# Optimization experiments

Measured on AMD Instinct MI355X. Metric: run time of the kernel, lower is better.

The kernel has to match this reference:

```python
import jax, jax.numpy as jnp
import numpy as np

N = 100000   # total nodes across all graphs
E = 1600000  # edges (avg degree 16)
D = 128      # input feature dim
H = 64       # hidden dim
B = 8        # number of graphs
EPS = 1e-5   # BatchNorm eps


def setup_inputs() -> dict:
    key = jax.random.key(0)
    ks = jax.random.split(key, 12)
    x = jax.random.normal(ks[0], (N, D), dtype=jnp.float32)
    edge_index = jax.random.randint(ks[1], (2, E), 0, N, dtype=jnp.int64)
    batch = jnp.sort(jax.random.randint(ks[2], (N,), 0, B, dtype=jnp.int64))
    s1 = 1.0 / np.sqrt(D)
    s2 = 1.0 / np.sqrt(H)
    W1l = jax.random.uniform(ks[3], (D, H), minval=-s1, maxval=s1, dtype=jnp.float32)
    W1r = jax.random.uniform(ks[4], (D, H), minval=-s1, maxval=s1, dtype=jnp.float32)
    b1 = jnp.zeros((H,), jnp.float32)
    gamma1 = jnp.ones((H,), jnp.float32)
    beta1 = jnp.zeros((H,), jnp.float32)
    W2l = jax.random.uniform(ks[5], (H, H), minval=-s2, maxval=s2, dtype=jnp.float32)
    W2r = jax.random.uniform(ks[6], (H, H), minval=-s2, maxval=s2, dtype=jnp.float32)
    b2 = jnp.zeros((H,), jnp.float32)
    return {"x": x, "edge_index": edge_index, "batch": batch,
            "W1l": W1l, "b1": b1, "W1r": W1r, "gamma1": gamma1, "beta1": beta1,
            "W2l": W2l, "b2": b2, "W2r": W2r}


def _seg_mean(vals, idx, num):
    # scatter-mean: sum per segment / count, zero-degree segments give 0 (count clamped)
    s = jax.ops.segment_sum(vals, idx, num_segments=num)
    cnt = jax.ops.segment_sum(jnp.ones((idx.shape[0], 1), vals.dtype), idx, num_segments=num)
    return s / jnp.maximum(cnt, 1.0)


def reference(x, edge_index, batch, W1l, b1, W1r, gamma1, beta1, W2l, b2, W2r):
    src, dst = edge_index[0], edge_index[1]
    # SAGEConv layer 1: mean-aggregate neighbors, lin_l(agg) + lin_r(x)
    agg1 = _seg_mean(x[src], dst, N)            # [N, D]
    h = agg1 @ W1l + b1 + x @ W1r               # [N, H]
    # BatchNorm1d (training-mode batch stats, biased var) then ReLU
    mu = jnp.mean(h, axis=0)
    var = jnp.var(h, axis=0)
    h = (h - mu) * jax.lax.rsqrt(var + EPS) * gamma1 + beta1
    h = jax.nn.relu(h)
    # SAGEConv layer 2 (no norm/act after last layer)
    agg2 = _seg_mean(h[src], dst, N)            # [N, H]
    h2 = agg2 @ W2l + b2 + h @ W2r              # [N, H]
    # per-graph global mean pool -> [B, H]
    return _seg_mean(h2, batch, B)
```

## Files before the change

kernel.cpp:

```cpp
#include <hip/hip_runtime.h>

#define N_NODES 100000
#define E_EDGES 1600000
#define DIM 128
#define HID 64
#define NGRAPH 8
#define EPSBN 1e-5f

#define GSHIFT 9
#define GNODES (1 << GSHIFT)
#define NGROUP ((N_NODES + GNODES - 1) >> GSHIFT)
#define GCAP 10240
#define CHUNK 2048
#define PBLK 256
#define EPT (CHUNK / PBLK)
#define NCHUNK ((E_EDGES + CHUNK - 1) / CHUNK)
#define MM1B ((N_NODES + 63) / 64)
#define GATB 2048

#if __has_builtin(__builtin_amdgcn_cvt_pk_fp8_f32) && \
    __has_builtin(__builtin_amdgcn_cvt_pk_f32_fp8)
#define HW_FP8 1
#else
#define HW_FP8 0
#endif

typedef float floatx2 __attribute__((ext_vector_type(2)));

__device__ __forceinline__ unsigned f2bf_pack(float lo, float hi) {
  unsigned ul = __float_as_uint(lo);
  unsigned uh = __float_as_uint(hi);
  ul = (ul + 0x7fffu + ((ul >> 16) & 1u)) >> 16;
  uh = (uh + 0x7fffu + ((uh >> 16) & 1u)) >> 16;
  return (uh << 16) | ul;
}
__device__ __forceinline__ float bflo(unsigned u) {
  return __uint_as_float(u << 16);
}
__device__ __forceinline__ float bfhi(unsigned u) {
  return __uint_as_float(u & 0xffff0000u);
}

#if !HW_FP8
__device__ __forceinline__ unsigned char f32_to_e4m3(float f) {
  unsigned u = __float_as_uint(f);
  unsigned s = (u >> 24) & 0x80u;
  float a = fabsf(f);
  if (a >= 464.f) return (unsigned char)(s | 0x7E);
  if (a < 0.015625f) {
    int m = (int)rintf(a * 512.f);
    if (m >= 8) return (unsigned char)(s | 0x08);
    return (unsigned char)(s | (unsigned)m);
  }
  int e = (int)((u >> 23) & 0xFF) - 127;
  float q = ldexpf(a, -e) * 8.f;
  int m = (int)rintf(q);
  if (m == 16) { m = 8; ++e; }
  if (e > 8) return (unsigned char)(s | 0x7E);
  return (unsigned char)(s | (unsigned)(((e + 7) << 3) | (m - 8)));
}
#endif

__device__ __forceinline__ unsigned pack4_e4m3(float a, float b, float c,
                                               float d) {
#if HW_FP8
  int w = __builtin_amdgcn_cvt_pk_fp8_f32(a, b, 0, false);
  w = __builtin_amdgcn_cvt_pk_fp8_f32(c, d, w, true);
  return (unsigned)w;
#else
  return (unsigned)f32_to_e4m3(a) | ((unsigned)f32_to_e4m3(b) << 8) |
         ((unsigned)f32_to_e4m3(c) << 16) | ((unsigned)f32_to_e4m3(d) << 24);
#endif
}

__global__ __launch_bounds__(PBLK) void part_mm1_kernel(
    const int* __restrict__ src, const int* __restrict__ dst,
    int* __restrict__ gcnt, unsigned* __restrict__ part,
    const float* __restrict__ x, const float* __restrict__ W1l,
    const float* __restrict__ W1r, unsigned char* __restrict__ y1f8,
    unsigned* __restrict__ y2bf) {
  __shared__ __align__(16) unsigned char smraw[32768];

  if (blockIdx.x < NCHUNK) {
    int* hist = (int*)(smraw);
    int* sc = (int*)(smraw + 1024);
    int* scanoff = (int*)(smraw + 2048);
    int* gbase = (int*)(smraw + 3072);
    unsigned* buf = (unsigned*)(smraw + 4096);
    unsigned char* gid = smraw + 12288;

    int c = blockIdx.x;
    int e0 = c * CHUNK;
    int m = E_EDGES - e0;
    m = m < CHUNK ? m : CHUNK;
    int t = threadIdx.x;

    hist[t] = 0;
    __syncthreads();

    int myg[EPT];
    unsigned mytok[EPT];
    int myrank[EPT];
    #pragma unroll
    for (int q = 0; q < EPT; ++q) {
      int i = t + q * PBLK;
      if (i < m) {
        int d = dst[e0 + i];
        int s = src[e0 + i];
        int g = d >> GSHIFT;
        myg[q] = g;
        mytok[q] = ((unsigned)(d & (GNODES - 1)) << 17) | (unsigned)s;
        myrank[q] = atomicAdd(&hist[g], 1);
      } else {
        myg[q] = -1;
      }
    }
    __syncthreads();

    sc[t] = hist[t];
    if (t < NGROUP && hist[t] > 0) gbase[t] = atomicAdd(&gcnt[t], hist[t]);
    __syncthreads();
    for (int off = 1; off < 256; off <<= 1) {
      int add = (t >= off) ? sc[t - off] : 0;
      __syncthreads();
      sc[t] += add;
      __syncthreads();
    }
    scanoff[t] = sc[t] - hist[t];
    __syncthreads();

    #pragma unroll
    for (int q = 0; q < EPT; ++q) {
      if (myg[q] >= 0) {
        int pos = scanoff[myg[q]] + myrank[q];
        buf[pos] = mytok[q];
        gid[pos] = (unsigned char)myg[q];
      }
    }
    __syncthreads();

    for (int i = t; i < m; i += PBLK) {
      int g = gid[i];
      int addr = gbase[g] + (i - scanoff[g]);
      if (addr < GCAP) part[(size_t)g * GCAP + addr] = buf[i];
    }
  } else {
    float* xlds = (float*)smraw;
    int t = threadIdx.x;
    int brow = (blockIdx.x - NCHUNK) * 64;

    for (int i = t; i < 64 * 32; i += PBLK) {
      int r = i >> 5;
      int c4 = (i & 31) << 2;
      int n = brow + r;
      if (n < N_NODES) {
        float4 v = *reinterpret_cast<const float4*>(x + (size_t)n * DIM + c4);
        int w = c4 ^ ((r & 7) << 2);
        *reinterpret_cast<float4*>(xlds + r * DIM + w) = v;
      }
    }
    __syncthreads();

    int lane = t & 63;
    int c0 = __builtin_amdgcn_readfirstlane((int)(t >> 6) << 4);
    int n = brow + lane;
    if (n >= N_NODES) return;
    const float* xr = xlds + lane * DIM;
    int sw = (lane & 7) << 2;

    float a1[16], a2[16];
    #pragma unroll
    for (int j = 0; j < 16; ++j) { a1[j] = 0.f; a2[j] = 0.f; }

    for (int k = 0; k < DIM; k += 4) {
      float4 xv = *reinterpret_cast<const float4*>(xr + (k ^ sw));
      float xs[4] = {xv.x, xv.y, xv.z, xv.w};
      #pragma unroll
      for (int kk = 0; kk < 4; ++kk) {
        const float* w1 = W1l + (size_t)(k + kk) * HID + c0;
        const float* w2 = W1r + (size_t)(k + kk) * HID + c0;
        float xk = xs[kk];
        #pragma unroll
        for (int j = 0; j < 16; ++j) {
          a1[j] = fmaf(xk, w1[j], a1[j]);
          a2[j] = fmaf(xk, w2[j], a2[j]);
        }
      }
    }
    uint4 pk;
    pk.x = pack4_e4m3(a1[0], a1[1], a1[2], a1[3]);
    pk.y = pack4_e4m3(a1[4], a1[5], a1[6], a1[7]);
    pk.z = pack4_e4m3(a1[8], a1[9], a1[10], a1[11]);
    pk.w = pack4_e4m3(a1[12], a1[13], a1[14], a1[15]);
    *reinterpret_cast<uint4*>(y1f8 + (size_t)n * HID + c0) = pk;

    uint4 q0, q1;
    q0.x = f2bf_pack(a2[0], a2[1]);
    q0.y = f2bf_pack(a2[2], a2[3]);
    q0.z = f2bf_pack(a2[4], a2[5]);
    q0.w = f2bf_pack(a2[6], a2[7]);
    q1.x = f2bf_pack(a2[8], a2[9]);
    q1.y = f2bf_pack(a2[10], a2[11]);
    q1.z = f2bf_pack(a2[12], a2[13]);
    q1.w = f2bf_pack(a2[14], a2[15]);
    unsigned* ob = y2bf + (size_t)n * (HID / 2) + (c0 >> 1);
    reinterpret_cast<uint4*>(ob)[0] = q0;
    reinterpret_cast<uint4*>(ob)[1] = q1;
  }
}

__global__ __launch_bounds__(512) void groupcsr_kernel(
    const int* __restrict__ gcnt, const unsigned* __restrict__ part,
    const int* __restrict__ batch, int* __restrict__ rowptr,
    int* __restrict__ csr, unsigned* __restrict__ tok2) {
  __shared__ int hist[GNODES];
  __shared__ int excl[GNODES];
  __shared__ int degl[GNODES];
  __shared__ int batl[GNODES];
  __shared__ int sc2[256];
  int g = blockIdx.x;
  int t = threadIdx.x;

  if (t < 256) sc2[t] = (t < NGROUP) ? min(gcnt[t], GCAP) : 0;
  __syncthreads();
  for (int off = 1; off < 256; off <<= 1) {
    int add = (t < 256 && t >= off) ? sc2[t - off] : 0;
    __syncthreads();
    if (t < 256) sc2[t] += add;
    __syncthreads();
  }
  int gbase = (g > 0) ? sc2[g - 1] : 0;

  hist[t] = 0;
  {
    int n = (g << GSHIFT) + t;
    batl[t] = (n < N_NODES) ? batch[n] : 0;
  }
  __syncthreads();

  int cnt = min(gcnt[g], GCAP);
  const unsigned* ga = part + (size_t)g * GCAP;
  for (int i = t; i < cnt; i += 512) atomicAdd(&hist[ga[i] >> 17], 1);
  __syncthreads();

  int orig = hist[t];
  degl[t] = orig;
  for (int off = 1; off < GNODES; off <<= 1) {
    int add = (t >= off) ? hist[t - off] : 0;
    __syncthreads();
    hist[t] += add;
    __syncthreads();
  }
  excl[t] = hist[t] - orig;
  __syncthreads();

  int n = (g << GSHIFT) + t;
  if (n <= N_NODES) rowptr[n] = gbase + excl[t];
  if (g == 0 && t == 0) rowptr[0] = 0;
  __syncthreads();

  for (int i = t; i < cnt; i += 512) {
    unsigned p = ga[i];
    int dloc = (int)(p >> 17);
    int pos = gbase + atomicAdd(&excl[dloc], 1);
    unsigned s = p & 0x1FFFFu;
    csr[pos] = (int)s;
    unsigned dg = (unsigned)degl[dloc];
    if (dg > 1023u) dg = 1023u;
    tok2[pos] = (dg << 20) | ((unsigned)batl[dloc] << 17) | s;
  }
}

__global__ __launch_bounds__(PBLK) void part2_gather_kernel(
    const unsigned* __restrict__ tok2, int* __restrict__ gcnt2,
    unsigned* __restrict__ part2, const uint2* __restrict__ yf8,
    const int* __restrict__ csr, const int* __restrict__ rowptr,
    const unsigned* __restrict__ otherbf, const float* __restrict__ bias,
    unsigned* __restrict__ outCbf, float* __restrict__ stats) {
  __shared__ int hist[256];
  __shared__ int sc[256];
  __shared__ int scanoff[256];
  __shared__ int gbase[256];
  __shared__ unsigned buf[CHUNK];
  __shared__ unsigned char gid[CHUNK];
  __shared__ float ss[HID];
  __shared__ float sq[HID];

  if (blockIdx.x < NCHUNK) {
    int c = blockIdx.x;
    int e0 = c * CHUNK;
    int m = E_EDGES - e0;
    m = m < CHUNK ? m : CHUNK;
    int t = threadIdx.x;

    hist[t] = 0;
    __syncthreads();

    int myg[EPT];
    unsigned mytok[EPT];
    int myrank[EPT];
    #pragma unroll
    for (int q = 0; q < EPT; ++q) {
      int i = t + q * PBLK;
      if (i < m) {
        unsigned p = tok2[e0 + i];
        int g = (int)((p & 0x1FFFFu) >> GSHIFT);
        myg[q] = g;
        mytok[q] = p;
        myrank[q] = atomicAdd(&hist[g], 1);
      } else {
        myg[q] = -1;
      }
    }
    __syncthreads();

    sc[t] = hist[t];
    if (t < NGROUP && hist[t] > 0) gbase[t] = atomicAdd(&gcnt2[t], hist[t]);
    __syncthreads();
    for (int off = 1; off < 256; off <<= 1) {
      int add = (t >= off) ? sc[t - off] : 0;
      __syncthreads();
      sc[t] += add;
      __syncthreads();
    }
    scanoff[t] = sc[t] - hist[t];
    __syncthreads();

    #pragma unroll
    for (int q = 0; q < EPT; ++q) {
      if (myg[q] >= 0) {
        int pos = scanoff[myg[q]] + myrank[q];
        buf[pos] = mytok[q];
        gid[pos] = (unsigned char)myg[q];
      }
    }
    __syncthreads();

    for (int i = t; i < m; i += PBLK) {
      int g = gid[i];
      int addr = gbase[g] + (i - scanoff[g]);
      if (addr < GCAP) part2[(size_t)g * GCAP + addr] = buf[i];
    }
  } else {
#if !HW_FP8
    __shared__ float tbl[256];
    {
      int t = threadIdx.x;
      if (t < 256) {
        int e = (t >> 3) & 15;
        int m = t & 7;
        float v = e ? ldexpf((float)(8 + m), e - 10) : ldexpf((float)m, -9);
        tbl[t] = (t & 0x80) ? -v : v;
      }
    }
    __syncthreads();
#endif
    int lane = threadIdx.x & 63;
    int oct = lane >> 3;
    int lo = lane & 7;
    int gbid = blockIdx.x - NCHUNK;
    int wid = (gbid * PBLK + (int)threadIdx.x) >> 6;
    const int nw = (GATB * PBLK) >> 6;

    float bj[8];
    #pragma unroll
    for (int k = 0; k < 8; ++k) bj[k] = bias[lo * 8 + k];

    float ls[8], lq[8];
    #pragma unroll
    for (int k = 0; k < 8; ++k) { ls[k] = 0.f; lq[k] = 0.f; }

    for (int nb = wid * 8; nb < N_NODES; nb += nw * 8) {
      int n = nb + oct;
      bool valid = n < N_NODES;
      int start = valid ? rowptr[n] : 0;
      int end = valid ? rowptr[n + 1] : 0;

      float acc[8];
      #pragma unroll
      for (int k = 0; k < 8; ++k) acc[k] = 0.f;

      for (int bse = start; bse < end; bse += 8) {
        int m = end - bse;
        m = m < 8 ? m : 8;
        int e = bse + lo;
        int s = (e < end) ? csr[e] : 0;
        uint2 vv[8];
        #pragma unroll
        for (int i = 0; i < 8; ++i) {
          int si = __shfl(s, i, 8);
          vv[i] = yf8[(size_t)si * 8 + lo];
        }
        #pragma unroll
        for (int i = 0; i < 8; ++i) {
          if (i < m) {
#if HW_FP8
            floatx2 p0 = __builtin_amdgcn_cvt_pk_f32_fp8((int)vv[i].x, false);
            floatx2 p1 = __builtin_amdgcn_cvt_pk_f32_fp8((int)vv[i].x, true);
            floatx2 p2 = __builtin_amdgcn_cvt_pk_f32_fp8((int)vv[i].y, false);
            floatx2 p3 = __builtin_amdgcn_cvt_pk_f32_fp8((int)vv[i].y, true);
            acc[0] += p0[0];
            acc[1] += p0[1];
            acc[2] += p1[0];
            acc[3] += p1[1];
            acc[4] += p2[0];
            acc[5] += p2[1];
            acc[6] += p3[0];
            acc[7] += p3[1];
#else
            acc[0] += tbl[vv[i].x & 255u];
            acc[1] += tbl[(vv[i].x >> 8) & 255u];
            acc[2] += tbl[(vv[i].x >> 16) & 255u];
            acc[3] += tbl[vv[i].x >> 24];
            acc[4] += tbl[vv[i].y & 255u];
            acc[5] += tbl[(vv[i].y >> 8) & 255u];
            acc[6] += tbl[(vv[i].y >> 16) & 255u];
            acc[7] += tbl[vv[i].y >> 24];
#endif
          }
        }
      }

      if (valid) {
        int deg = end - start;
        float inv = 1.f / (float)(deg > 1 ? deg : 1);
        uint4 ov = *reinterpret_cast<const uint4*>(otherbf +
                                                   (size_t)n * (HID / 2) +
                                                   lo * 4);
        float v[8];
        v[0] = fmaf(acc[0], inv, bj[0]) + bflo(ov.x);
        v[1] = fmaf(acc[1], inv, bj[1]) + bfhi(ov.x);
        v[2] = fmaf(acc[2], inv, bj[2]) + bflo(ov.y);
        v[3] = fmaf(acc[3], inv, bj[3]) + bfhi(ov.y);
        v[4] = fmaf(acc[4], inv, bj[4]) + bflo(ov.z);
        v[5] = fmaf(acc[5], inv, bj[5]) + bfhi(ov.z);
        v[6] = fmaf(acc[6], inv, bj[6]) + bflo(ov.w);
        v[7] = fmaf(acc[7], inv, bj[7]) + bfhi(ov.w);
        uint4 cw4;
        cw4.x = f2bf_pack(v[0], v[1]);
        cw4.y = f2bf_pack(v[2], v[3]);
        cw4.z = f2bf_pack(v[4], v[5]);
        cw4.w = f2bf_pack(v[6], v[7]);
        *reinterpret_cast<uint4*>(outCbf + (size_t)n * (HID / 2) + lo * 4) =
            cw4;
        #pragma unroll
        for (int k = 0; k < 8; ++k) {
          ls[k] += v[k];
          lq[k] = fmaf(v[k], v[k], lq[k]);
        }
      }
    }

    int t = threadIdx.x;
    if (t < HID) { ss[t] = 0.f; sq[t] = 0.f; }
    __syncthreads();
    #pragma unroll
    for (int k = 0; k < 8; ++k) {
      atomicAdd(&ss[lo * 8 + k], ls[k]);
      atomicAdd(&sq[lo * 8 + k], lq[k]);
    }
    __syncthreads();
    if (t < HID) {
      unsafeAtomicAdd(&stats[t], ss[t]);
      unsafeAtomicAdd(&stats[HID + t], sq[t]);
    }
  }
}

__global__ __launch_bounds__(256) void chsum_kernel(
    const int* __restrict__ gcnt2, const unsigned* __restrict__ part2,
    const unsigned* __restrict__ Cbf, const float* __restrict__ stats,
    const float* __restrict__ gamma, const float* __restrict__ beta,
    const int* __restrict__ batch, float* __restrict__ S1g,
    float* __restrict__ S2g) {
  __shared__ float c[GNODES * NGRAPH];
  __shared__ float r1[HID * NGRAPH];
  __shared__ float r2[HID * NGRAPH];
  int g = blockIdx.x;
  int t = threadIdx.x;

  for (int i = t; i < GNODES * NGRAPH; i += 256) c[i] = 0.f;
  for (int i = t; i < HID * NGRAPH; i += 256) { r1[i] = 0.f; r2[i] = 0.f; }
  __syncthreads();

  int cnt = min(gcnt2[g], GCAP);
  const unsigned* ga = part2 + (size_t)g * GCAP;
  for (int i = t; i < cnt; i += 256) {
    unsigned p = ga[i];
    int sl = (int)(p & (GNODES - 1));
    int b = (int)((p >> 17) & 7u);
    int deg = (int)((p >> 20) & 0x3FFu);
    float w = 1.f / (float)(deg > 1 ? deg : 1);
    atomicAdd(&c[sl * NGRAPH + b], w);
  }
  __syncthreads();

  int lane = t & 63;
  int wv = t >> 6;

  float inv_n = 1.0f / (float)N_NODES;
  float mu = stats[lane] * inv_n;
  float var = stats[HID + lane] * inv_n - mu * mu;
  float scl = gamma[lane] * rsqrtf(var + EPSBN);
  float shf = beta[lane] - mu * scl;

  float s1[NGRAPH], s2[NGRAPH];
  #pragma unroll
  for (int b = 0; b < NGRAPH; ++b) { s1[b] = 0.f; s2[b] = 0.f; }

  int nend = N_NODES - (g << GSHIFT);
  nend = nend < GNODES ? nend : GNODES;
  for (int nl = wv; nl < nend; nl += 4) {
    int n = (g << GSHIFT) + nl;
    unsigned u = Cbf[(size_t)n * (HID / 2) + (lane >> 1)];
    float hr = (lane & 1) ? bfhi(u) : bflo(u);
    float h = fmaf(hr, scl, shf);
    h = h > 0.f ? h : 0.f;
    int bn = batch[n];
    #pragma unroll
    for (int b = 0; b < NGRAPH; ++b) {
      float cb = c[nl * NGRAPH + b];
      s1[b] = fmaf(cb, h, s1[b]);
      s2[b] += (b == bn) ? h : 0.f;
    }
  }

  #pragma unroll
  for (int b = 0; b < NGRAPH; ++b) {
    atomicAdd(&r1[b * HID + lane], s1[b]);
    atomicAdd(&r2[b * HID + lane], s2[b]);
  }
  __syncthreads();
  for (int i = t; i < HID * NGRAPH; i += 256) {
    unsafeAtomicAdd(&S1g[i], r1[i]);
    unsafeAtomicAdd(&S2g[i], r2[i]);
  }
}

__device__ __forceinline__ int lbound(const int* __restrict__ a, int key) {
  int lo = 0, hi = N_NODES;
  while (lo < hi) {
    int mid = (lo + hi) >> 1;
    if (a[mid] < key) lo = mid + 1; else hi = mid;
  }
  return lo;
}

__global__ __launch_bounds__(512) void finale_kernel(
    const float* __restrict__ S1g, const float* __restrict__ S2g,
    const int* __restrict__ batch, const float* __restrict__ W2l,
    const float* __restrict__ W2r, const float* __restrict__ b2,
    float* __restrict__ out) {
  int t = threadIdx.x;
  int b = t >> 6;
  int oc = t & 63;
  int V = lbound(batch, b + 1) - lbound(batch, b);
  float acc = 0.f;
  for (int k = 0; k < HID; ++k) {
    acc = fmaf(S1g[b * HID + k], W2l[k * HID + oc], acc);
    acc = fmaf(S2g[b * HID + k], W2r[k * HID + oc], acc);
  }
  out[t] = (V > 0) ? (acc / (float)V + b2[oc]) : 0.f;
}

extern "C" void kernel_launch(void* const* d_in, const int* in_sizes, int n_in,
                              void* d_out, int out_size, void* d_ws,
                              size_t ws_size, hipStream_t stream) {
  const float* x      = (const float*)d_in[0];
  const int*   ei     = (const int*)d_in[1];
  const int*   batch  = (const int*)d_in[2];
  const float* W1l    = (const float*)d_in[3];
  const float* b1     = (const float*)d_in[4];
  const float* W1r    = (const float*)d_in[5];
  const float* gamma1 = (const float*)d_in[6];
  const float* beta1  = (const float*)d_in[7];
  const float* W2l    = (const float*)d_in[8];
  const float* b2     = (const float*)d_in[9];
  const float* W2r    = (const float*)d_in[10];

  const int* src = ei;
  const int* dst = ei + E_EDGES;

  float* ws = (float*)d_ws;
  size_t off = 0;
  unsigned char* Af8 = (unsigned char*)(ws + off);
  off += (size_t)N_NODES * HID / 4;
  unsigned* Bbf = (unsigned*)(ws + off);
  off += (size_t)N_NODES * (HID / 2);
  unsigned* Cbf = (unsigned*)(ws + off);
  off += (size_t)N_NODES * (HID / 2);
  int* gcnt     = (int*)(ws + off); off += 256;
  int* gcnt2    = (int*)(ws + off); off += 256;
  float* stats  = ws + off; off += 2 * HID;
  float* S1g    = ws + off; off += NGRAPH * HID;
  float* S2g    = ws + off; off += NGRAPH * HID;
  size_t zero_elems = 256 + 256 + 2 * HID + 2 * NGRAPH * HID;
  int* rowptr   = (int*)(ws + off); off += N_NODES + 1;
  int* csr      = (int*)(ws + off); off += E_EDGES;
  unsigned* tok2 = (unsigned*)(ws + off); off += E_EDGES;
  unsigned* part = (unsigned*)(ws + off); off += (size_t)NGROUP * GCAP;

  hipMemsetAsync(gcnt, 0, zero_elems * sizeof(float), stream);

  part_mm1_kernel<<<NCHUNK + MM1B, PBLK, 0, stream>>>(
      src, dst, gcnt, part, x, W1l, W1r, Af8, Bbf);

  groupcsr_kernel<<<NGROUP, 512, 0, stream>>>(gcnt, part, batch, rowptr, csr,
                                              tok2);

  part2_gather_kernel<<<NCHUNK + GATB, PBLK, 0, stream>>>(
      tok2, gcnt2, part, (const uint2*)Af8, csr, rowptr, Bbf, b1, Cbf, stats);

  chsum_kernel<<<NGROUP, 256, 0, stream>>>(gcnt2, part, Cbf, stats, gamma1,
                                           beta1, batch, S1g, S2g);

  finale_kernel<<<1, 512, 0, stream>>>(S1g, S2g, batch, W2l, W2r, b2,
                                       (float*)d_out);
}
```

Measured before the change: 272.7 us.

## Compute first-layer projections with bf16 MFMA and pre-transposed weights

Replaces the scalar FMA loop that multiplied x by W1l and W1r with bf16 MFMA 16x16x32 instructions. A small new kernel converts and transposes both weight matrices to bf16 once per call, and each block stages the x tile and the weights in padded shared memory. Results go back through shared memory before the existing fp8/bf16 packing and stores. The intent is to cut ALU time in the matmul blocks. In exchange it adds a kernel launch, makes the shared-memory footprint larger (which may lower occupancy for the partition blocks), and rounds x to bf16 before the product.

New measurement: 242.4 us. -11.1%, faster.

```diff
diff --git a/kernel.cpp b/kernel.cpp
--- a/kernel.cpp
+++ b/kernel.cpp
@@ -26,6 +26,8 @@
 #endif
 
 typedef float floatx2 __attribute__((ext_vector_type(2)));
+typedef short bf16x8 __attribute__((ext_vector_type(8)));
+typedef float f32x4 __attribute__((ext_vector_type(4)));
 
 __device__ __forceinline__ unsigned f2bf_pack(float lo, float hi) {
   unsigned ul = __float_as_uint(lo);
@@ -73,13 +75,23 @@
 #endif
 }
 
+__global__ __launch_bounds__(64) void wprep_kernel(
+    const float* __restrict__ W1l, const float* __restrict__ W1r,
+    unsigned* __restrict__ wTbf) {
+  int n = blockIdx.x;
+  int kp = threadIdx.x;
+  const float* Wc = (n < 64) ? (W1l + n) : (W1r + (n - 64));
+  float w0 = Wc[(size_t)(2 * kp) * HID];
+  float w1 = Wc[(size_t)(2 * kp + 1) * HID];
+  wTbf[n * 64 + kp] = f2bf_pack(w0, w1);
+}
+
 __global__ __launch_bounds__(PBLK) void part_mm1_kernel(
     const int* __restrict__ src, const int* __restrict__ dst,
     int* __restrict__ gcnt, unsigned* __restrict__ part,
-    const float* __restrict__ x, const float* __restrict__ W1l,
-    const float* __restrict__ W1r, unsigned char* __restrict__ y1f8,
-    unsigned* __restrict__ y2bf) {
-  __shared__ __align__(16) unsigned char smraw[32768];
+    const float* __restrict__ x, const unsigned* __restrict__ wTbf,
+    unsigned char* __restrict__ y1f8, unsigned* __restrict__ y2bf) {
+  __shared__ __align__(16) unsigned char smraw[52224];
 
   if (blockIdx.x < NCHUNK) {
     int* hist = (int*)(smraw);
@@ -145,7 +157,8 @@
       if (addr < GCAP) part[(size_t)g * GCAP + addr] = buf[i];
     }
   } else {
-    float* xlds = (float*)smraw;
+    short* xs = (short*)smraw;
+    short* wts = (short*)(smraw + 17408);
     int t = threadIdx.x;
     int brow = (blockIdx.x - NCHUNK) * 64;
 
@@ -153,59 +166,82 @@
       int r = i >> 5;
       int c4 = (i & 31) << 2;
       int n = brow + r;
+      unsigned lo = 0u, hi = 0u;
       if (n < N_NODES) {
         float4 v = *reinterpret_cast<const float4*>(x + (size_t)n * DIM + c4);
-        int w = c4 ^ ((r & 7) << 2);
-        *reinterpret_cast<float4*>(xlds + r * DIM + w) = v;
-      }
+        lo = f2bf_pack(v.x, v.y);
+        hi = f2bf_pack(v.z, v.w);
+      }
+      unsigned* dp = (unsigned*)(xs + r * 136 + c4);
+      dp[0] = lo;
+      dp[1] = hi;
+    }
+    for (int i = t; i < 128 * 64; i += PBLK) {
+      int nn = i >> 6;
+      int kp = i & 63;
+      *(unsigned*)(wts + nn * 136 + kp * 2) = wTbf[i];
     }
     __syncthreads();
 
     int lane = t & 63;
-    int c0 = __builtin_amdgcn_readfirstlane((int)(t >> 6) << 4);
-    int n = brow + lane;
-    if (n >= N_NODES) return;
-    const float* xr = xlds + lane * DIM;
-    int sw = (lane & 7) << 2;
-
-    float a1[16], a2[16];
-    #pragma unroll
-    for (int j = 0; j < 16; ++j) { a1[j] = 0.f; a2[j] = 0.f; }
-
-    for (int k = 0; k < DIM; k += 4) {
-      float4 xv = *reinterpret_cast<const float4*>(xr + (k ^ sw));
-      float xs[4] = {xv.x, xv.y, xv.z, xv.w};
+    int w = t >> 6;
+    int l15 = lane & 15;
+    int lg = lane >> 4;
+
+    f32x4 acc[8];
+    #pragma unroll
+    for (int j = 0; j < 8; ++j) acc[j] = (f32x4){0.f, 0.f, 0.f, 0.f};
+
+    #pragma unroll
+    for (int ks = 0; ks < 4; ++ks) {
+      int k0 = ks * 32 + lg * 8;
+      bf16x8 a = *(const bf16x8*)(xs + (w * 16 + l15) * 136 + k0);
       #pragma unroll
-      for (int kk = 0; kk < 4; ++kk) {
-        const float* w1 = W1l + (size_t)(k + kk) * HID + c0;
-        const float* w2 = W1r + (size_t)(k + kk) * HID + c0;
-        float xk = xs[kk];
-        #pragma unroll
-        for (int j = 0; j < 16; ++j) {
-          a1[j] = fmaf(xk, w1[j], a1[j]);
-          a2[j] = fmaf(xk, w2[j], a2[j]);
-        }
-      }
-    }
-    uint4 pk;
-    pk.x = pack4_e4m3(a1[0], a1[1], a1[2], a1[3]);
-    pk.y = pack4_e4m3(a1[4], a1[5], a1[6], a1[7]);
-    pk.z = pack4_e4m3(a1[8], a1[9], a1[10], a1[11]);
-    pk.w = pack4_e4m3(a1[12], a1[13], a1[14], a1[15]);
-    *reinterpret_cast<uint4*>(y1f8 + (size_t)n * HID + c0) = pk;
-
-    uint4 q0, q1;
-    q0.x = f2bf_pack(a2[0], a2[1]);
-    q0.y = f2bf_pack(a2[2], a2[3]);
-    q0.z = f2bf_pack(a2[4], a2[5]);
-    q0.w = f2bf_pack(a2[6], a2[7]);
-    q1.x = f2bf_pack(a2[8], a2[9]);
-    q1.y = f2bf_pack(a2[10], a2[11]);
-    q1.z = f2bf_pack(a2[12], a2[13]);
-    q1.w = f2bf_pack(a2[14], a2[15]);
-    unsigned* ob = y2bf + (size_t)n * (HID / 2) + (c0 >> 1);
-    reinterpret_cast<uint4*>(ob)[0] = q0;
-    reinterpret_cast<uint4*>(ob)[1] = q1;
+      for (int nf = 0; nf < 8; ++nf) {
+        bf16x8 b = *(const bf16x8*)(wts + (nf * 16 + l15) * 136 + k0);
+        acc[nf] =
+            __builtin_amdgcn_mfma_f32_16x16x32_bf16(a, b, acc[nf], 0, 0, 0);
+      }
+    }
+    __syncthreads();
+
+    float* osm = (float*)smraw;
+    #pragma unroll
+    for (int nf = 0; nf < 8; ++nf) {
+      int col = nf * 16 + l15;
+      int r0 = w * 16 + lg * 4;
+      #pragma unroll
+      for (int rg = 0; rg < 4; ++rg)
+        osm[(r0 + rg) * 132 + col] = acc[nf][rg];
+    }
+    __syncthreads();
+
+    int r = t & 63;
+    int cq = (t >> 6) << 4;
+    int n = brow + r;
+    if (n < N_NODES) {
+      const float* a1 = osm + r * 132 + cq;
+      const float* a2 = osm + r * 132 + 64 + cq;
+      uint4 pk;
+      pk.x = pack4_e4m3(a1[0], a1[1], a1[2], a1[3]);
+      pk.y = pack4_e4m3(a1[4], a1[5], a1[6], a1[7]);
+      pk.z = pack4_e4m3(a1[8], a1[9], a1[10], a1[11]);
+      pk.w = pack4_e4m3(a1[12], a1[13], a1[14], a1[15]);
+      *reinterpret_cast<uint4*>(y1f8 + (size_t)n * HID + cq) = pk;
+
+      uint4 q0, q1;
+      q0.x = f2bf_pack(a2[0], a2[1]);
+      q0.y = f2bf_pack(a2[2], a2[3]);
+      q0.z = f2bf_pack(a2[4], a2[5]);
+      q0.w = f2bf_pack(a2[6], a2[7]);
+      q1.x = f2bf_pack(a2[8], a2[9]);
+      q1.y = f2bf_pack(a2[10], a2[11]);
+      q1.z = f2bf_pack(a2[12], a2[13]);
+      q1.w = f2bf_pack(a2[14], a2[15]);
+      unsigned* ob = y2bf + (size_t)n * (HID / 2) + (cq >> 1);
+      reinterpret_cast<uint4*>(ob)[0] = q0;
+      reinterpret_cast<uint4*>(ob)[1] = q1;
+    }
   }
 }
 
@@ -595,6 +631,7 @@
   float* S1g    = ws + off; off += NGRAPH * HID;
   float* S2g    = ws + off; off += NGRAPH * HID;
   size_t zero_elems = 256 + 256 + 2 * HID + 2 * NGRAPH * HID;
+  unsigned* wTbf = (unsigned*)(ws + off); off += 128 * 64;
   int* rowptr   = (int*)(ws + off); off += N_NODES + 1;
   int* csr      = (int*)(ws + off); off += E_EDGES;
   unsigned* tok2 = (unsigned*)(ws + off); off += E_EDGES;
@@ -602,8 +639,10 @@
 
   hipMemsetAsync(gcnt, 0, zero_elems * sizeof(float), stream);
 
+  wprep_kernel<<<128, 64, 0, stream>>>(W1l, W1r, wTbf);
+
   part_mm1_kernel<<<NCHUNK + MM1B, PBLK, 0, stream>>>(
-      src, dst, gcnt, part, x, W1l, W1r, Af8, Bbf);
+      src, dst, gcnt, part, x, wTbf, Af8, Bbf);
 
   groupcsr_kernel<<<NGROUP, 512, 0, stream>>>(gcnt, part, batch, rowptr, csr,
                                               tok2);
```
